# Optimization experiments

Measured on AMD Instinct MI355X. Metric: run time of the kernel, lower is better.

## Reference

```python
import jax, jax.numpy as jnp
import numpy as np

N = 4096
IN_F = 512
OUT_F = 64
N_HEADS = 8
ALPHA = 0.2
NEG_INF = -9e15


def setup_inputs() -> dict:
    key = jax.random.key(0)
    k1, k2, k3, k4 = jax.random.split(key, 4)
    h = jax.random.normal(k1, (N, IN_F), dtype=jnp.float32)
    adj = jax.random.randint(k2, (N, N), 0, 2, dtype=jnp.int32)
    W = jax.random.normal(k3, (IN_F, OUT_F * N_HEADS), dtype=jnp.float32) * (1.414 / np.sqrt(IN_F))
    a = jax.random.normal(k4, (2 * OUT_F, 1), dtype=jnp.float32) * 0.1
    return {"h": h, "adj": adj, "W": W, "a": a}


def reference(h, adj, W, a):
    # Wh: [N, H, F]
    Wh = (h @ W).reshape(N, N_HEADS, OUT_F)
    # The all-pairs concat + matmul with a ([2F,1], shared across heads)
    # decomposes exactly: e[i,j,h] = leakyrelu(Wh[i,h]@a[:F] + Wh[j,h]@a[F:])
    a_src = a[:OUT_F, 0]
    a_dst = a[OUT_F:, 0]
    src = jnp.einsum('nhf,f->nh', Wh, a_src)  # [N, H]
    dst = jnp.einsum('nhf,f->nh', Wh, a_dst)  # [N, H]
    e = src[:, None, :] + dst[None, :, :]      # [N, N, H]
    e = jnp.where(e > 0, e, ALPHA * e)         # leaky relu
    e = jnp.where(adj[:, :, None] > 0, e, NEG_INF)
    attention = jax.nn.softmax(e, axis=1)      # softmax over neighbors j
    h_prime = jnp.einsum('ijh,jhf->ihf', attention, Wh)  # [N, H, F]
    out = h_prime.reshape(N, N_HEADS * OUT_F)
    return jax.nn.elu(out)
```

## Files before the change

### kernel.cpp

```cpp
#include <hip/hip_runtime.h>
#include <hip/hip_bf16.h>


typedef unsigned short ushort_t;
typedef __attribute__((ext_vector_type(8))) short bf16x8;
typedef __attribute__((ext_vector_type(4))) float f32x4;

#define LOG2E 1.4426950408889634f

__device__ __forceinline__ ushort_t f2bf(float x) {
    unsigned u = __builtin_bit_cast(unsigned, x);
    u += 0x7FFFu + ((u >> 16) & 1u);
    return (ushort_t)(u >> 16);
}

__global__ __launch_bounds__(256) void transpose_w(const float* __restrict__ W,
                                                   ushort_t* __restrict__ WT) {
    __shared__ ushort_t t[32][33];
    int bx = blockIdx.x & 15, by = blockIdx.x >> 4;
    int tx = threadIdx.x & 31, ty = threadIdx.x >> 5;
#pragma unroll
    for (int i = 0; i < 32; i += 8)
        t[ty + i][tx] = f2bf(W[(by * 32 + ty + i) * 512 + bx * 32 + tx]);
    __syncthreads();
#pragma unroll
    for (int i = 0; i < 32; i += 8)
        WT[(bx * 32 + ty + i) * 512 + by * 32 + tx] = t[tx][ty + i];
}

__global__ __launch_bounds__(256) void gemm_whT(const ushort_t* __restrict__ WT,
                                                const float* __restrict__ h,
                                                const float* __restrict__ a,
                                                ushort_t* __restrict__ WhT,
                                                float* __restrict__ expA,
                                                float* __restrict__ expC,
                                                float* __restrict__ expB,
                                                float* __restrict__ expD) {
    __shared__ ushort_t Al[64][40];
    __shared__ ushort_t Bl[64][40];
    __shared__ float asrc[64], adst[64];
    __shared__ float sred[2][4][64];
    int tid = threadIdx.x;
    int wave = tid >> 6, lane = tid & 63, quad = lane >> 4, nn = lane & 15;
    int mb = blockIdx.x & 7, nb = blockIdx.x >> 3;
    if (tid < 64) {
        asrc[tid] = a[tid] * LOG2E;
        adst[tid] = a[64 + tid] * LOG2E;
    }
    int r = tid >> 2, part = tid & 3;
    const ushort_t* Ag = WT + (unsigned)((mb * 64 + r) * 512 + part * 8);
    const float* Bg = h + (unsigned)((nb * 64 + r) * 512 + part * 8);
    f32x4 acc[4] = {};
    for (int kb = 0; kb < 512; kb += 32) {
        __syncthreads();
        *(bf16x8*)&Al[r][part * 8] = *(const bf16x8*)(Ag + kb);
        float4 f0 = *(const float4*)(Bg + kb);
        float4 f1 = *(const float4*)(Bg + kb + 4);
        bf16x8 bvv;
        bvv[0] = (short)f2bf(f0.x); bvv[1] = (short)f2bf(f0.y);
        bvv[2] = (short)f2bf(f0.z); bvv[3] = (short)f2bf(f0.w);
        bvv[4] = (short)f2bf(f1.x); bvv[5] = (short)f2bf(f1.y);
        bvv[6] = (short)f2bf(f1.z); bvv[7] = (short)f2bf(f1.w);
        *(bf16x8*)&Bl[r][part * 8] = bvv;
        __syncthreads();
        bf16x8 af = *(const bf16x8*)&Al[wave * 16 + nn][quad * 8];
#pragma unroll
        for (int nt = 0; nt < 4; nt++) {
            bf16x8 bv = *(const bf16x8*)&Bl[nt * 16 + nn][quad * 8];
            acc[nt] = __builtin_amdgcn_mfma_f32_16x16x32_bf16(af, bv, acc[nt], 0, 0, 0);
        }
    }
    int row0 = mb * 64 + wave * 16 + quad * 4;
    int col0 = nb * 64 + nn;
    int f0i = wave * 16 + quad * 4;
#pragma unroll
    for (int nt = 0; nt < 4; nt++) {
        float s = 0.f, d = 0.f;
#pragma unroll
        for (int rr = 0; rr < 4; rr++) {
            float v = acc[nt][rr];
            WhT[(unsigned)((row0 + rr) * 4096 + col0 + nt * 16)] = f2bf(v);
            s += v * asrc[f0i + rr];
            d += v * adst[f0i + rr];
        }
        s += __shfl_xor(s, 16); s += __shfl_xor(s, 32);
        d += __shfl_xor(d, 16); d += __shfl_xor(d, 32);
        if (quad == 0) { sred[0][wave][nt * 16 + nn] = s; sred[1][wave][nt * 16 + nn] = d; }
    }
    __syncthreads();
    if (tid < 64) {
        float s = sred[0][0][tid] + sred[0][1][tid] + sred[0][2][tid] + sred[0][3][tid];
        unsigned idx = mb * 4096 + nb * 64 + tid;
        expA[idx] = __builtin_amdgcn_exp2f(s);
        expC[idx] = __builtin_amdgcn_exp2f(0.2f * s);
    } else if (tid < 128) {
        int c = tid - 64;
        float d = sred[1][0][c] + sred[1][1][c] + sred[1][2][c] + sred[1][3][c];
        unsigned idx = mb * 4096 + nb * 64 + c;
        expB[idx] = __builtin_amdgcn_exp2f(d);
        expD[idx] = __builtin_amdgcn_exp2f(0.2f * d);
    }
}

__global__ __launch_bounds__(512, 4) void gat_attn(const int* __restrict__ adj,
                                                   const ushort_t* __restrict__ WhT,
                                                   const float* __restrict__ expA,
                                                   const float* __restrict__ expC,
                                                   const float* __restrict__ expB,
                                                   const float* __restrict__ expD,
                                                   float* __restrict__ out) {
    __shared__ __align__(16) ushort_t Vb[2][128][72];
    __shared__ __align__(16) ushort_t Pb[2][2][32][72];
    __shared__ float denoml[2][32];
    int tid = threadIdx.x;
    int wave = tid >> 6, lane = tid & 63, quad = lane >> 4, nn = lane & 15;
    int hb = blockIdx.x >> 7, ib = blockIdx.x & 127;
    int i0 = ib * 32;
    int hh = tid >> 8, tt = tid & 255;
    int pi = tt >> 3, jo = tt & 7;
    int head = hb * 2 + hh;
    float Ai = expA[head * 4096 + i0 + pi];
    float Ci = expC[head * 4096 + i0 + pi];
    const int* adjP = adj + (unsigned)(i0 + pi) * 4096 + jo * 8;
    const float* Bp = expB + (unsigned)head * 4096 + jo * 8;
    const float* Dp = expD + (unsigned)head * 4096 + jo * 8;
    int vr = tid >> 3, vcs = tid & 7;
    const ushort_t* Vg0 = WhT + (unsigned)(hb * 128 + vr) * 4096 + vcs * 8;
    const ushort_t* Vg1 = Vg0 + 64u * 4096u;
    int jhalf = wave >> 2, ws = wave & 3;
    int strip = ws & 1, whead = ws >> 1;
    f32x4 acc[4] = {};
    float dpart = 0.f;
    int4 pa[2][2]; bf16x8 pvv[2][2];
    pa[0][0] = *(const int4*)(adjP);
    pa[0][1] = *(const int4*)(adjP + 4);
    pvv[0][0] = *(const bf16x8*)(Vg0);
    pvv[0][1] = *(const bf16x8*)(Vg1);
#pragma unroll 2
    for (int k = 0; k < 64; k++) {
        int cb = k & 1;
        float4 Bv0 = *(const float4*)(Bp + k * 64);
        float4 Bv1 = *(const float4*)(Bp + k * 64 + 4);
        float4 Dv0 = *(const float4*)(Dp + k * 64);
        float4 Dv1 = *(const float4*)(Dp + k * 64 + 4);
        int4 a0 = pa[cb][0], a1 = pa[cb][1];
        unsigned w0, w1, w2, w3, w4, w5, w6, w7;
        {
            float w;
            w = fmaxf(Ai * Bv0.x, Ci * Dv0.x);
            w0 = __builtin_bit_cast(unsigned, w) & 0xFFFF0000u;  w0 = a0.x > 0 ? w0 : 0u;
            w = fmaxf(Ai * Bv0.y, Ci * Dv0.y);
            w1 = __builtin_bit_cast(unsigned, w) & 0xFFFF0000u;  w1 = a0.y > 0 ? w1 : 0u;
            w = fmaxf(Ai * Bv0.z, Ci * Dv0.z);
            w2 = __builtin_bit_cast(unsigned, w) & 0xFFFF0000u;  w2 = a0.z > 0 ? w2 : 0u;
            w = fmaxf(Ai * Bv0.w, Ci * Dv0.w);
            w3 = __builtin_bit_cast(unsigned, w) & 0xFFFF0000u;  w3 = a0.w > 0 ? w3 : 0u;
            w = fmaxf(Ai * Bv1.x, Ci * Dv1.x);
            w4 = __builtin_bit_cast(unsigned, w) & 0xFFFF0000u;  w4 = a1.x > 0 ? w4 : 0u;
            w = fmaxf(Ai * Bv1.y, Ci * Dv1.y);
            w5 = __builtin_bit_cast(unsigned, w) & 0xFFFF0000u;  w5 = a1.y > 0 ? w5 : 0u;
            w = fmaxf(Ai * Bv1.z, Ci * Dv1.z);
            w6 = __builtin_bit_cast(unsigned, w) & 0xFFFF0000u;  w6 = a1.z > 0 ? w6 : 0u;
            w = fmaxf(Ai * Bv1.w, Ci * Dv1.w);
            w7 = __builtin_bit_cast(unsigned, w) & 0xFFFF0000u;  w7 = a1.w > 0 ? w7 : 0u;
        }
        dpart += __builtin_bit_cast(float, w0) + __builtin_bit_cast(float, w1)
               + __builtin_bit_cast(float, w2) + __builtin_bit_cast(float, w3)
               + __builtin_bit_cast(float, w4) + __builtin_bit_cast(float, w5)
               + __builtin_bit_cast(float, w6) + __builtin_bit_cast(float, w7);
        uint4 pq;
        pq.x = __builtin_amdgcn_perm(w1, w0, 0x07060302u);
        pq.y = __builtin_amdgcn_perm(w3, w2, 0x07060302u);
        pq.z = __builtin_amdgcn_perm(w5, w4, 0x07060302u);
        pq.w = __builtin_amdgcn_perm(w7, w6, 0x07060302u);
        *(uint4*)&Pb[cb][hh][pi][jo * 8] = pq;
        *(bf16x8*)&Vb[cb][vr][vcs * 8] = pvv[cb][0];
        *(bf16x8*)&Vb[cb][64 + vr][vcs * 8] = pvv[cb][1];
        if (k < 63) {
            const int* ap = adjP + (k + 1) * 64;
            pa[cb ^ 1][0] = *(const int4*)(ap);
            pa[cb ^ 1][1] = *(const int4*)(ap + 4);
            pvv[cb ^ 1][0] = *(const bf16x8*)(Vg0 + (k + 1) * 64);
            pvv[cb ^ 1][1] = *(const bf16x8*)(Vg1 + (k + 1) * 64);
        }
        if (k > 0) {
            int pbuf = cb ^ 1;
            bf16x8 af = *(const bf16x8*)&Pb[pbuf][whead][strip * 16 + nn][jhalf * 32 + quad * 8];
#pragma unroll
            for (int nt = 0; nt < 4; nt++) {
                bf16x8 bv = *(const bf16x8*)&Vb[pbuf][whead * 64 + nt * 16 + nn][jhalf * 32 + quad * 8];
                acc[nt] = __builtin_amdgcn_mfma_f32_16x16x32_bf16(af, bv, acc[nt], 0, 0, 0);
            }
        }
        __syncthreads();
    }
    {
        bf16x8 af = *(const bf16x8*)&Pb[1][whead][strip * 16 + nn][jhalf * 32 + quad * 8];
#pragma unroll
        for (int nt = 0; nt < 4; nt++) {
            bf16x8 bv = *(const bf16x8*)&Vb[1][whead * 64 + nt * 16 + nn][jhalf * 32 + quad * 8];
            acc[nt] = __builtin_amdgcn_mfma_f32_16x16x32_bf16(af, bv, acc[nt], 0, 0, 0);
        }
    }
    float dsum = dpart;
    dsum += __shfl_xor(dsum, 1);
    dsum += __shfl_xor(dsum, 2);
    dsum += __shfl_xor(dsum, 4);
    if ((tid & 7) == 0) denoml[hh][pi] = dsum;
    __syncthreads();
    float (*cmb)[64][8] = reinterpret_cast<float (*)[64][8]>(&Vb[0][0][0]);
    if (jhalf == 1) {
        *(f32x4*)&cmb[ws][lane][0] = acc[0] ;
        *(f32x4*)&cmb[ws][lane][4] = acc[1];
    }
    __syncthreads();
    if (jhalf == 0) {
        f32x4 o0 = acc[0] + *(const f32x4*)&cmb[ws][lane][0];
        f32x4 o1 = acc[1] + *(const f32x4*)&cmb[ws][lane][4];
#pragma unroll
        for (int rr = 0; rr < 4; rr++) {
            int il = strip * 16 + quad * 4 + rr;
            float dnm = fmaxf(denoml[whead][il], 1e-30f);
            float v0 = o0[rr] / dnm;
            float v1 = o1[rr] / dnm;
            v0 = v0 > 0.f ? v0 : __expf(v0) - 1.f;
            v1 = v1 > 0.f ? v1 : __expf(v1) - 1.f;
            unsigned oi = (unsigned)(i0 + il) * 512 + hb * 128 + whead * 64 + nn;
            out[oi] = v0;
            out[oi + 16] = v1;
        }
    }
    __syncthreads();
    if (jhalf == 1) {
        *(f32x4*)&cmb[ws][lane][0] = acc[2];
        *(f32x4*)&cmb[ws][lane][4] = acc[3];
    }
    __syncthreads();
    if (jhalf == 0) {
        f32x4 o0 = acc[2] + *(const f32x4*)&cmb[ws][lane][0];
        f32x4 o1 = acc[3] + *(const f32x4*)&cmb[ws][lane][4];
#pragma unroll
        for (int rr = 0; rr < 4; rr++) {
            int il = strip * 16 + quad * 4 + rr;
            float dnm = fmaxf(denoml[whead][il], 1e-30f);
            float v0 = o0[rr] / dnm;
            float v1 = o1[rr] / dnm;
            v0 = v0 > 0.f ? v0 : __expf(v0) - 1.f;
            v1 = v1 > 0.f ? v1 : __expf(v1) - 1.f;
            unsigned oi = (unsigned)(i0 + il) * 512 + hb * 128 + whead * 64 + 32 + nn;
            out[oi] = v0;
            out[oi + 16] = v1;
        }
    }
}

extern "C" void kernel_launch(void* const* d_in, const int* in_sizes, int n_in,
                              void* d_out, int out_size, void* d_ws, size_t ws_size,
                              hipStream_t stream) {
    const float* h   = (const float*)d_in[0];
    const int*   adj = (const int*)d_in[1];
    const float* W   = (const float*)d_in[2];
    const float* a   = (const float*)d_in[3];

    char* ws = (char*)d_ws;
    ushort_t* WhT = (ushort_t*)ws;
    ushort_t* WT  = (ushort_t*)(ws + (4u << 20));
    float* expA = (float*)(ws + (4u << 20) + (512u << 10));
    float* expC = expA + 8 * 4096;
    float* expB = expC + 8 * 4096;
    float* expD = expB + 8 * 4096;

    transpose_w<<<256, 256, 0, stream>>>(W, WT);
    gemm_whT<<<512, 256, 0, stream>>>(WT, h, a, WhT, expA, expC, expB, expD);
    gat_attn<<<512, 512, 0, stream>>>(adj, WhT, expA, expC, expB, expD,
                                      (float*)d_out);
}
```

Measured before the change: 200.7 us.

## Double-buffer GEMM shared tiles and prefetch attention B/D exponent loads

```diff
diff --git a/kernel.cpp b/kernel.cpp
--- a/kernel.cpp
+++ b/kernel.cpp
@@ -28,16 +28,16 @@
         WT[(bx * 32 + ty + i) * 512 + by * 32 + tx] = t[tx][ty + i];
 }
 
-__global__ __launch_bounds__(256) void gemm_whT(const ushort_t* __restrict__ WT,
-                                                const float* __restrict__ h,
-                                                const float* __restrict__ a,
-                                                ushort_t* __restrict__ WhT,
-                                                float* __restrict__ expA,
-                                                float* __restrict__ expC,
-                                                float* __restrict__ expB,
-                                                float* __restrict__ expD) {
-    __shared__ ushort_t Al[64][40];
-    __shared__ ushort_t Bl[64][40];
+__global__ __launch_bounds__(256, 4) void gemm_whT(const ushort_t* __restrict__ WT,
+                                                   const float* __restrict__ h,
+                                                   const float* __restrict__ a,
+                                                   ushort_t* __restrict__ WhT,
+                                                   float* __restrict__ expA,
+                                                   float* __restrict__ expC,
+                                                   float* __restrict__ expB,
+                                                   float* __restrict__ expD) {
+    __shared__ __align__(16) ushort_t Al[2][64][72];
+    __shared__ __align__(16) ushort_t Bl[2][64][72];
     __shared__ float asrc[64], adst[64];
     __shared__ float sred[2][4][64];
     int tid = threadIdx.x;
@@ -47,27 +47,64 @@
         asrc[tid] = a[tid] * LOG2E;
         adst[tid] = a[64 + tid] * LOG2E;
     }
-    int r = tid >> 2, part = tid & 3;
-    const ushort_t* Ag = WT + (unsigned)((mb * 64 + r) * 512 + part * 8);
-    const float* Bg = h + (unsigned)((nb * 64 + r) * 512 + part * 8);
+    int r = tid >> 2, s0 = tid & 3;
+    const ushort_t* Ag = WT + (unsigned)((mb * 64 + r) * 512 + s0 * 8);
+    const float* Bg = h + (unsigned)((nb * 64 + r) * 512 + s0 * 8);
+    bf16x8 pA0 = *(const bf16x8*)(Ag);
+    bf16x8 pA1 = *(const bf16x8*)(Ag + 32);
+    float4 pb0 = *(const float4*)(Bg);
+    float4 pb1 = *(const float4*)(Bg + 4);
+    float4 pb2 = *(const float4*)(Bg + 32);
+    float4 pb3 = *(const float4*)(Bg + 36);
     f32x4 acc[4] = {};
-    for (int kb = 0; kb < 512; kb += 32) {
+#pragma unroll 2
+    for (int t = 0; t < 8; t++) {
+        int cb = t & 1;
+        *(bf16x8*)&Al[cb][r][s0 * 8] = pA0;
+        *(bf16x8*)&Al[cb][r][s0 * 8 + 32] = pA1;
+        bf16x8 bv;
+        bv[0] = (short)f2bf(pb0.x); bv[1] = (short)f2bf(pb0.y);
+        bv[2] = (short)f2bf(pb0.z); bv[3] = (short)f2bf(pb0.w);
+        bv[4] = (short)f2bf(pb1.x); bv[5] = (short)f2bf(pb1.y);
+        bv[6] = (short)f2bf(pb1.z); bv[7] = (short)f2bf(pb1.w);
+        *(bf16x8*)&Bl[cb][r][s0 * 8] = bv;
+        bv[0] = (short)f2bf(pb2.x); bv[1] = (short)f2bf(pb2.y);
+        bv[2] = (short)f2bf(pb2.z); bv[3] = (short)f2bf(pb2.w);
+        bv[4] = (short)f2bf(pb3.x); bv[5] = (short)f2bf(pb3.y);
+        bv[6] = (short)f2bf(pb3.z); bv[7] = (short)f2bf(pb3.w);
+        *(bf16x8*)&Bl[cb][r][s0 * 8 + 32] = bv;
+        if (t < 7) {
+            int ko = (t + 1) * 64;
+            pA0 = *(const bf16x8*)(Ag + ko);
+            pA1 = *(const bf16x8*)(Ag + ko + 32);
+            pb0 = *(const float4*)(Bg + ko);
+            pb1 = *(const float4*)(Bg + ko + 4);
+            pb2 = *(const float4*)(Bg + ko + 32);
+            pb3 = *(const float4*)(Bg + ko + 36);
+        }
+        if (t > 0) {
+            int pb = cb ^ 1;
+            bf16x8 af0 = *(const bf16x8*)&Al[pb][wave * 16 + nn][quad * 8];
+            bf16x8 af1 = *(const bf16x8*)&Al[pb][wave * 16 + nn][32 + quad * 8];
+#pragma unroll
+            for (int nt = 0; nt < 4; nt++) {
+                bf16x8 b0 = *(const bf16x8*)&Bl[pb][nt * 16 + nn][quad * 8];
+                bf16x8 b1 = *(const bf16x8*)&Bl[pb][nt * 16 + nn][32 + quad * 8];
+                acc[nt] = __builtin_amdgcn_mfma_f32_16x16x32_bf16(af0, b0, acc[nt], 0, 0, 0);
+                acc[nt] = __builtin_amdgcn_mfma_f32_16x16x32_bf16(af1, b1, acc[nt], 0, 0, 0);
+            }
+        }
         __syncthreads();
-        *(bf16x8*)&Al[r][part * 8] = *(const bf16x8*)(Ag + kb);
-        float4 f0 = *(const float4*)(Bg + kb);
-        float4 f1 = *(const float4*)(Bg + kb + 4);
-        bf16x8 bvv;
-        bvv[0] = (short)f2bf(f0.x); bvv[1] = (short)f2bf(f0.y);
-        bvv[2] = (short)f2bf(f0.z); bvv[3] = (short)f2bf(f0.w);
-        bvv[4] = (short)f2bf(f1.x); bvv[5] = (short)f2bf(f1.y);
-        bvv[6] = (short)f2bf(f1.z); bvv[7] = (short)f2bf(f1.w);
-        *(bf16x8*)&Bl[r][part * 8] = bvv;
-        __syncthreads();
-        bf16x8 af = *(const bf16x8*)&Al[wave * 16 + nn][quad * 8];
+    }
+    {
+        bf16x8 af0 = *(const bf16x8*)&Al[1][wave * 16 + nn][quad * 8];
+        bf16x8 af1 = *(const bf16x8*)&Al[1][wave * 16 + nn][32 + quad * 8];
 #pragma unroll
         for (int nt = 0; nt < 4; nt++) {
-            bf16x8 bv = *(const bf16x8*)&Bl[nt * 16 + nn][quad * 8];
-            acc[nt] = __builtin_amdgcn_mfma_f32_16x16x32_bf16(af, bv, acc[nt], 0, 0, 0);
+            bf16x8 b0 = *(const bf16x8*)&Bl[1][nt * 16 + nn][quad * 8];
+            bf16x8 b1 = *(const bf16x8*)&Bl[1][nt * 16 + nn][32 + quad * 8];
+            acc[nt] = __builtin_amdgcn_mfma_f32_16x16x32_bf16(af0, b0, acc[nt], 0, 0, 0);
+            acc[nt] = __builtin_amdgcn_mfma_f32_16x16x32_bf16(af1, b1, acc[nt], 0, 0, 0);
         }
     }
     int row0 = mb * 64 + wave * 16 + quad * 4;
@@ -131,18 +168,20 @@
     int strip = ws & 1, whead = ws >> 1;
     f32x4 acc[4] = {};
     float dpart = 0.f;
-    int4 pa[2][2]; bf16x8 pvv[2][2];
+    int4 pa[2][2]; bf16x8 pvv[2][2]; float4 pBD[2][4];
     pa[0][0] = *(const int4*)(adjP);
     pa[0][1] = *(const int4*)(adjP + 4);
     pvv[0][0] = *(const bf16x8*)(Vg0);
     pvv[0][1] = *(const bf16x8*)(Vg1);
+    pBD[0][0] = *(const float4*)(Bp);
+    pBD[0][1] = *(const float4*)(Bp + 4);
+    pBD[0][2] = *(const float4*)(Dp);
+    pBD[0][3] = *(const float4*)(Dp + 4);
 #pragma unroll 2
     for (int k = 0; k < 64; k++) {
         int cb = k & 1;
-        float4 Bv0 = *(const float4*)(Bp + k * 64);
-        float4 Bv1 = *(const float4*)(Bp + k * 64 + 4);
-        float4 Dv0 = *(const float4*)(Dp + k * 64);
-        float4 Dv1 = *(const float4*)(Dp + k * 64 + 4);
+        float4 Bv0 = pBD[cb][0], Bv1 = pBD[cb][1];
+        float4 Dv0 = pBD[cb][2], Dv1 = pBD[cb][3];
         int4 a0 = pa[cb][0], a1 = pa[cb][1];
         unsigned w0, w1, w2, w3, w4, w5, w6, w7;
         {
@@ -180,6 +219,10 @@
             const int* ap = adjP + (k + 1) * 64;
             pa[cb ^ 1][0] = *(const int4*)(ap);
             pa[cb ^ 1][1] = *(const int4*)(ap + 4);
+            pBD[cb ^ 1][0] = *(const float4*)(Bp + (k + 1) * 64);
+            pBD[cb ^ 1][1] = *(const float4*)(Bp + (k + 1) * 64 + 4);
+            pBD[cb ^ 1][2] = *(const float4*)(Dp + (k + 1) * 64);
+            pBD[cb ^ 1][3] = *(const float4*)(Dp + (k + 1) * 64 + 4);
             pvv[cb ^ 1][0] = *(const bf16x8*)(Vg0 + (k + 1) * 64);
             pvv[cb ^ 1][1] = *(const bf16x8*)(Vg1 + (k + 1) * 64);
         }
@@ -210,7 +253,7 @@
     __syncthreads();
     float (*cmb)[64][8] = reinterpret_cast<float (*)[64][8]>(&Vb[0][0][0]);
     if (jhalf == 1) {
-        *(f32x4*)&cmb[ws][lane][0] = acc[0] ;
+        *(f32x4*)&cmb[ws][lane][0] = acc[0];
         *(f32x4*)&cmb[ws][lane][4] = acc[1];
     }
     __syncthreads();
```

After: 191.4 us. 1.05x faster.
